# Kernel tuning notes

Hardware: AMD Instinct MI355X
Metric: run time of the kernel (lower is better)

## Reference

```python
import jax, jax.numpy as jnp
import numpy as np

D = 448  # state_dim == input_dim == output_dim

def _param(key, shape):
    # matches torch.rand(shape) * 0.1 + 0.001
    return jax.random.uniform(key, shape, dtype=jnp.float32) * 0.1 + 0.001

def setup_inputs() -> dict:
    key = jax.random.key(0)
    ks = jax.random.split(key, 9)
    x = jax.random.normal(ks[0], (8, 4096, D), dtype=jnp.float32)
    return {
        "x": x,
        "W_q": _param(ks[1], (D, D)),
        "W_k": _param(ks[2], (D, D)),
        "W_v": _param(ks[3], (D, D)),
        "W_o": _param(ks[4], (D, D)),
        "SSM_A": _param(ks[5], (D, D)),
        "SSM_B": _param(ks[6], (D, D)),
        "SSM_C": _param(ks[7], (D, D)),
    }

def reference(x, W_q, W_k, W_v, W_o, SSM_A, SSM_B, SSM_C):
    # seq_len=4096 > threshold=256 -> quadratic SSM path.
    # structured_processing's einsum 'bsd,dd->bsd' multiplies elementwise by
    # the diagonal of the matrix; the block loop is redundant, so we apply the
    # diagonal scale over the whole sequence in one fused op.
    q = jnp.einsum('bsi,id->bsd', x, W_q)
    k = jnp.einsum('bsi,id->bsd', x, W_k)
    v = jnp.einsum('bsi,id->bsd', x, W_v)
    ssm = (q * jnp.diagonal(SSM_A)
           + k * jnp.diagonal(SSM_B)
           + v * jnp.diagonal(SSM_C))
    # dropout is identity in eval mode
    return jnp.einsum('bsd,do->bso', ssm, W_o)
```

## Files before the change

### kernel.cpp

```cpp
#include <hip/hip_runtime.h>
#include <hip/hip_bf16.h>

#define DDIM 448
#define NSTEP 14

typedef __hip_bfloat16 bf16;
typedef __attribute__((ext_vector_type(8))) short short8;
typedef __attribute__((ext_vector_type(4))) float f32x4;

__device__ __forceinline__ short bf_bits(float f) {
    bf16 h = __float2bfloat16(f);
    return *reinterpret_cast<short*>(&h);
}

__device__ __forceinline__ void async16(const bf16* g, bf16* l) {
    __builtin_amdgcn_global_load_lds(
        (const __attribute__((address_space(1))) void*)g,
        (__attribute__((address_space(3))) void*)l, 16, 0, 0);
}

__global__ __launch_bounds__(256) void prep_wc(
    const float* __restrict__ Wq, const float* __restrict__ Wk,
    const float* __restrict__ Wv, const float* __restrict__ Wo,
    const float* __restrict__ Ad, const float* __restrict__ Bd,
    const float* __restrict__ Cd, bf16* __restrict__ Wt)
{
    __shared__ __align__(16) bf16 As[64 * 32];
    __shared__ __align__(16) bf16 Bs[64 * 32];
    __shared__ float da[DDIM], db[DDIM], dc[DDIM];

    const int tid  = threadIdx.x;
    const int i0   = blockIdx.x * 64;
    const int o0   = blockIdx.y * 64;
    const int lane = tid & 63;
    const int wid  = tid >> 6;
    const int wm   = wid >> 1, wn = wid & 1;
    const int m_   = lane & 15, kq = lane >> 4;

    for (int d = tid; d < DDIM; d += 256) {
        da[d] = Ad[d * DDIM + d];
        db[d] = Bd[d * DDIM + d];
        dc[d] = Cd[d * DDIM + d];
    }

    const int dr  = tid >> 3;
    const int oc8 = (tid & 7) * 8;
    const int ir  = tid >> 2;
    const int dc8 = (tid & 3) * 8;

    f32x4 acc[2][2] = {};

    f32x4 w0 = *(const f32x4*)(Wo + dr * DDIM + o0 + oc8);
    f32x4 w1 = *(const f32x4*)(Wo + dr * DDIM + o0 + oc8 + 4);
    f32x4 q0 = *(const f32x4*)(Wq + (i0 + ir) * DDIM + dc8);
    f32x4 q1 = *(const f32x4*)(Wq + (i0 + ir) * DDIM + dc8 + 4);
    f32x4 t0 = *(const f32x4*)(Wk + (i0 + ir) * DDIM + dc8);
    f32x4 t1 = *(const f32x4*)(Wk + (i0 + ir) * DDIM + dc8 + 4);
    f32x4 v0 = *(const f32x4*)(Wv + (i0 + ir) * DDIM + dc8);
    f32x4 v1 = *(const f32x4*)(Wv + (i0 + ir) * DDIM + dc8 + 4);

    for (int k0 = 0; k0 < DDIM; k0 += 32) {
        __syncthreads();
        #pragma unroll
        for (int j = 0; j < 4; ++j) {
            As[(oc8 + j) * 32 + dr]     = __float2bfloat16(w0[j]);
            As[(oc8 + 4 + j) * 32 + dr] = __float2bfloat16(w1[j]);
        }
        short8 e;
        #pragma unroll
        for (int j = 0; j < 4; ++j) {
            e[j]     = bf_bits(q0[j] * da[k0 + dc8 + j]
                             + t0[j] * db[k0 + dc8 + j]
                             + v0[j] * dc[k0 + dc8 + j]);
            e[j + 4] = bf_bits(q1[j] * da[k0 + dc8 + 4 + j]
                             + t1[j] * db[k0 + dc8 + 4 + j]
                             + v1[j] * dc[k0 + dc8 + 4 + j]);
        }
        *(short8*)&Bs[ir * 32 + dc8] = e;
        __syncthreads();

        const int kn = (k0 + 32 < DDIM) ? k0 + 32 : 0;
        w0 = *(const f32x4*)(Wo + (kn + dr) * DDIM + o0 + oc8);
        w1 = *(const f32x4*)(Wo + (kn + dr) * DDIM + o0 + oc8 + 4);
        q0 = *(const f32x4*)(Wq + (i0 + ir) * DDIM + kn + dc8);
        q1 = *(const f32x4*)(Wq + (i0 + ir) * DDIM + kn + dc8 + 4);
        t0 = *(const f32x4*)(Wk + (i0 + ir) * DDIM + kn + dc8);
        t1 = *(const f32x4*)(Wk + (i0 + ir) * DDIM + kn + dc8 + 4);
        v0 = *(const f32x4*)(Wv + (i0 + ir) * DDIM + kn + dc8);
        v1 = *(const f32x4*)(Wv + (i0 + ir) * DDIM + kn + dc8 + 4);

        short8 af[2], bfr[2];
        #pragma unroll
        for (int mi = 0; mi < 2; ++mi)
            af[mi] = *(const short8*)&As[(wm * 32 + mi * 16 + m_) * 32 + kq * 8];
        #pragma unroll
        for (int ni = 0; ni < 2; ++ni)
            bfr[ni] = *(const short8*)&Bs[(wn * 32 + ni * 16 + m_) * 32 + kq * 8];
        #pragma unroll
        for (int mi = 0; mi < 2; ++mi)
            #pragma unroll
            for (int ni = 0; ni < 2; ++ni)
                acc[mi][ni] = __builtin_amdgcn_mfma_f32_16x16x32_bf16(
                    af[mi], bfr[ni], acc[mi][ni], 0, 0, 0);
    }

    #pragma unroll
    for (int mi = 0; mi < 2; ++mi)
        #pragma unroll
        for (int ni = 0; ni < 2; ++ni) {
            const int o = o0 + wm * 32 + mi * 16 + kq * 4;
            const int i = i0 + wn * 32 + ni * 16 + m_;
            bf16* dst = Wt + (i >> 5) * (DDIM * 32) + (i & 31);
            #pragma unroll
            for (int r = 0; r < 4; ++r)
                dst[(o + r) * 32] = __float2bfloat16(acc[mi][ni][r]);
        }
}

__global__ __launch_bounds__(256, 1) void gemm_xwc(
    const float* __restrict__ X, const bf16* __restrict__ Wt,
    float* __restrict__ out)
{
    __shared__ __align__(16) char smem[74240];

    const int tid  = threadIdx.x;
    const int lane = tid & 63;
    const int wid  = tid >> 6;
    const int m_   = lane & 15;
    const int kq   = lane >> 4;
    const int row0 = blockIdx.x * 128;

    const int ar = tid >> 1;
    const int ac = (tid & 1) * 16;
    const float* agp = X + (row0 + ar) * DDIM + ac;

    const bf16* bgp = Wt + wid * 7 * 512 + lane * 8;

    f32x4 acc[8][7] = {};

    {
        bf16* B0 = (bf16*)(smem + 16384);
        #pragma unroll
        for (int j = 0; j < 7; ++j)
            async16(bgp + j * 512, B0 + (wid * 7 + j) * 512);
    }

    f32x4 a0 = *(const f32x4*)(agp);
    f32x4 a1 = *(const f32x4*)(agp + 4);
    f32x4 a2 = *(const f32x4*)(agp + 8);
    f32x4 a3 = *(const f32x4*)(agp + 12);
    {
        bf16* A0 = (bf16*)smem;
        short8 w0, w1;
        #pragma unroll
        for (int j = 0; j < 4; ++j) {
            w0[j] = bf_bits(a0[j]); w0[j + 4] = bf_bits(a1[j]);
            w1[j] = bf_bits(a2[j]); w1[j + 4] = bf_bits(a3[j]);
        }
        *(short8*)&A0[ar * 32 + ac]     = w0;
        *(short8*)&A0[ar * 32 + ac + 8] = w1;
    }
    a0 = *(const f32x4*)(agp + 32);
    a1 = *(const f32x4*)(agp + 36);
    a2 = *(const f32x4*)(agp + 40);
    a3 = *(const f32x4*)(agp + 44);
    __syncthreads();

    for (int s = 0; s < NSTEP; ++s) {
        const int cur = s & 1, nxt = cur ^ 1;
        const bf16* Ac = (const bf16*)(smem + (cur << 13));
        const bf16* Bc = (const bf16*)(smem + 16384 + cur * 28672);

        if (s + 1 < NSTEP) {
            bf16* An = (bf16*)(smem + (nxt << 13));
            bf16* Bn = (bf16*)(smem + 16384 + nxt * 28672);
            short8 w0, w1;
            #pragma unroll
            for (int j = 0; j < 4; ++j) {
                w0[j] = bf_bits(a0[j]); w0[j + 4] = bf_bits(a1[j]);
                w1[j] = bf_bits(a2[j]); w1[j + 4] = bf_bits(a3[j]);
            }
            *(short8*)&An[ar * 32 + ac]     = w0;
            *(short8*)&An[ar * 32 + ac + 8] = w1;
            const bf16* bsrc = bgp + (s + 1) * (DDIM * 32);
            #pragma unroll
            for (int j = 0; j < 7; ++j)
                async16(bsrc + j * 512, Bn + (wid * 7 + j) * 512);
            if (s + 2 < NSTEP) {
                const int k2 = (s + 2) * 32;
                a0 = *(const f32x4*)(agp + k2);
                a1 = *(const f32x4*)(agp + k2 + 4);
                a2 = *(const f32x4*)(agp + k2 + 8);
                a3 = *(const f32x4*)(agp + k2 + 12);
            }
        }

        short8 af[8], bfr[7];
        #pragma unroll
        for (int mi = 0; mi < 8; ++mi)
            af[mi] = *(const short8*)&Ac[(mi * 16 + m_) * 32 + kq * 8];
        #pragma unroll
        for (int ni = 0; ni < 7; ++ni)
            bfr[ni] = *(const short8*)&Bc[(wid * 112 + ni * 16 + m_) * 32 + kq * 8];

        #pragma unroll
        for (int mi = 0; mi < 8; ++mi)
            #pragma unroll
            for (int ni = 0; ni < 7; ++ni)
                acc[mi][ni] = __builtin_amdgcn_mfma_f32_16x16x32_bf16(
                    af[mi], bfr[ni], acc[mi][ni], 0, 0, 0);

        __syncthreads();
    }

    float* Cb = (float*)(smem + 16384);
    #pragma unroll
    for (int t = 0; t < 4; ++t) {
        #pragma unroll
        for (int mi2 = 0; mi2 < 2; ++mi2) {
            const int mi = t * 2 + mi2;
            #pragma unroll
            for (int ni = 0; ni < 7; ++ni) {
                const int col = wid * 112 + ni * 16 + m_;
                #pragma unroll
                for (int r = 0; r < 4; ++r)
                    Cb[(mi2 * 16 + kq * 4 + r) * 452 + col] = acc[mi][ni][r];
            }
        }
        __syncthreads();
        const f32x4* Cb4 = (const f32x4*)Cb;
        f32x4* dst4 = (f32x4*)(out + (row0 + t * 32) * DDIM);
        #pragma unroll
        for (int j = 0; j < 14; ++j) {
            const int v   = j * 256 + tid;
            const int row = v / 112;
            const int cw  = v - row * 112;
            dst4[v] = Cb4[row * 113 + cw];
        }
        __syncthreads();
    }
}

extern "C" void kernel_launch(void* const* d_in, const int* in_sizes, int n_in,
                              void* d_out, int out_size, void* d_ws, size_t ws_size,
                              hipStream_t stream) {
    const float* x  = (const float*)d_in[0];
    const float* Wq = (const float*)d_in[1];
    const float* Wk = (const float*)d_in[2];
    const float* Wv = (const float*)d_in[3];
    const float* Wo = (const float*)d_in[4];
    const float* Ad = (const float*)d_in[5];
    const float* Bd = (const float*)d_in[6];
    const float* Cd = (const float*)d_in[7];

    bf16*  Wt  = (bf16*)d_ws;
    float* out = (float*)d_out;

    const int M = in_sizes[0] / DDIM;

    prep_wc<<<dim3(7, 7), 256, 0, stream>>>(Wq, Wk, Wv, Wo, Ad, Bd, Cd, Wt);
    gemm_xwc<<<M / 128, 256, 0, stream>>>(x, Wt, out);
}
```

Measured before the change: 145.1 us.

## Split GEMM tile across 8 waves with 512-thread blocks

```diff
diff --git a/kernel.cpp b/kernel.cpp
--- a/kernel.cpp
+++ b/kernel.cpp
@@ -117,7 +117,7 @@
         }
 }
 
-__global__ __launch_bounds__(256, 1) void gemm_xwc(
+__global__ __launch_bounds__(512, 2) void gemm_xwc(
     const float* __restrict__ X, const bf16* __restrict__ Wt,
     float* __restrict__ out)
 {
@@ -126,44 +126,42 @@
     const int tid  = threadIdx.x;
     const int lane = tid & 63;
     const int wid  = tid >> 6;
+    const int wr   = wid >> 2;
+    const int wc   = wid & 3;
     const int m_   = lane & 15;
     const int kq   = lane >> 4;
     const int row0 = blockIdx.x * 128;
 
-    const int ar = tid >> 1;
-    const int ac = (tid & 1) * 16;
+    const int ar = tid >> 2;
+    const int ac = (tid & 3) * 8;
     const float* agp = X + (row0 + ar) * DDIM + ac;
 
-    const bf16* bgp = Wt + wid * 7 * 512 + lane * 8;
-
-    f32x4 acc[8][7] = {};
+    const bf16* bgp = Wt + wc * 7 * 512 + lane * 8;
+
+    f32x4 acc[4][7] = {};
 
     {
         bf16* B0 = (bf16*)(smem + 16384);
-        #pragma unroll
-        for (int j = 0; j < 7; ++j)
-            async16(bgp + j * 512, B0 + (wid * 7 + j) * 512);
+        if (wid < 4) {
+            #pragma unroll
+            for (int j = 0; j < 7; ++j)
+                async16(bgp + j * 512, B0 + (wc * 7 + j) * 512);
+        }
     }
 
     f32x4 a0 = *(const f32x4*)(agp);
     f32x4 a1 = *(const f32x4*)(agp + 4);
-    f32x4 a2 = *(const f32x4*)(agp + 8);
-    f32x4 a3 = *(const f32x4*)(agp + 12);
     {
         bf16* A0 = (bf16*)smem;
-        short8 w0, w1;
+        short8 w;
         #pragma unroll
         for (int j = 0; j < 4; ++j) {
-            w0[j] = bf_bits(a0[j]); w0[j + 4] = bf_bits(a1[j]);
-            w1[j] = bf_bits(a2[j]); w1[j + 4] = bf_bits(a3[j]);
-        }
-        *(short8*)&A0[ar * 32 + ac]     = w0;
-        *(short8*)&A0[ar * 32 + ac + 8] = w1;
+            w[j] = bf_bits(a0[j]); w[j + 4] = bf_bits(a1[j]);
+        }
+        *(short8*)&A0[ar * 32 + ac] = w;
     }
     a0 = *(const f32x4*)(agp + 32);
     a1 = *(const f32x4*)(agp + 36);
-    a2 = *(const f32x4*)(agp + 40);
-    a3 = *(const f32x4*)(agp + 44);
     __syncthreads();
 
     for (int s = 0; s < NSTEP; ++s) {
@@ -174,37 +172,35 @@
         if (s + 1 < NSTEP) {
             bf16* An = (bf16*)(smem + (nxt << 13));
             bf16* Bn = (bf16*)(smem + 16384 + nxt * 28672);
-            short8 w0, w1;
+            short8 w;
             #pragma unroll
             for (int j = 0; j < 4; ++j) {
-                w0[j] = bf_bits(a0[j]); w0[j + 4] = bf_bits(a1[j]);
-                w1[j] = bf_bits(a2[j]); w1[j + 4] = bf_bits(a3[j]);
-            }
-            *(short8*)&An[ar * 32 + ac]     = w0;
-            *(short8*)&An[ar * 32 + ac + 8] = w1;
-            const bf16* bsrc = bgp + (s + 1) * (DDIM * 32);
-            #pragma unroll
-            for (int j = 0; j < 7; ++j)
-                async16(bsrc + j * 512, Bn + (wid * 7 + j) * 512);
+                w[j] = bf_bits(a0[j]); w[j + 4] = bf_bits(a1[j]);
+            }
+            *(short8*)&An[ar * 32 + ac] = w;
+            if (wid < 4) {
+                const bf16* bsrc = bgp + (s + 1) * (DDIM * 32);
+                #pragma unroll
+                for (int j = 0; j < 7; ++j)
+                    async16(bsrc + j * 512, Bn + (wc * 7 + j) * 512);
+            }
             if (s + 2 < NSTEP) {
                 const int k2 = (s + 2) * 32;
                 a0 = *(const f32x4*)(agp + k2);
                 a1 = *(const f32x4*)(agp + k2 + 4);
-                a2 = *(const f32x4*)(agp + k2 + 8);
-                a3 = *(const f32x4*)(agp + k2 + 12);
-            }
-        }
-
-        short8 af[8], bfr[7];
-        #pragma unroll
-        for (int mi = 0; mi < 8; ++mi)
-            af[mi] = *(const short8*)&Ac[(mi * 16 + m_) * 32 + kq * 8];
+            }
+        }
+
+        short8 af[4], bfr[7];
+        #pragma unroll
+        for (int mi = 0; mi < 4; ++mi)
+            af[mi] = *(const short8*)&Ac[(wr * 64 + mi * 16 + m_) * 32 + kq * 8];
         #pragma unroll
         for (int ni = 0; ni < 7; ++ni)
-            bfr[ni] = *(const short8*)&Bc[(wid * 112 + ni * 16 + m_) * 32 + kq * 8];
-
-        #pragma unroll
-        for (int mi = 0; mi < 8; ++mi)
+            bfr[ni] = *(const short8*)&Bc[(wc * 112 + ni * 16 + m_) * 32 + kq * 8];
+
+        #pragma unroll
+        for (int mi = 0; mi < 4; ++mi)
             #pragma unroll
             for (int ni = 0; ni < 7; ++ni)
                 acc[mi][ni] = __builtin_amdgcn_mfma_f32_16x16x32_bf16(
@@ -216,23 +212,25 @@
     float* Cb = (float*)(smem + 16384);
     #pragma unroll
     for (int t = 0; t < 4; ++t) {
-        #pragma unroll
-        for (int mi2 = 0; mi2 < 2; ++mi2) {
-            const int mi = t * 2 + mi2;
-            #pragma unroll
-            for (int ni = 0; ni < 7; ++ni) {
-                const int col = wid * 112 + ni * 16 + m_;
+        if (wr == (t >> 1)) {
+            #pragma unroll
+            for (int mi2 = 0; mi2 < 2; ++mi2) {
+                const int mi = (t & 1) * 2 + mi2;
                 #pragma unroll
-                for (int r = 0; r < 4; ++r)
-                    Cb[(mi2 * 16 + kq * 4 + r) * 452 + col] = acc[mi][ni][r];
+                for (int ni = 0; ni < 7; ++ni) {
+                    const int col = wc * 112 + ni * 16 + m_;
+                    #pragma unroll
+                    for (int r = 0; r < 4; ++r)
+                        Cb[(mi2 * 16 + kq * 4 + r) * 452 + col] = acc[mi][ni][r];
+                }
             }
         }
         __syncthreads();
         const f32x4* Cb4 = (const f32x4*)Cb;
         f32x4* dst4 = (f32x4*)(out + (row0 + t * 32) * DDIM);
         #pragma unroll
-        for (int j = 0; j < 14; ++j) {
-            const int v   = j * 256 + tid;
+        for (int j = 0; j < 7; ++j) {
+            const int v   = j * 512 + tid;
             const int row = v / 112;
             const int cw  = v - row * 112;
             dst4[v] = Cb4[row * 113 + cw];
@@ -259,5 +257,5 @@
     const int M = in_sizes[0] / DDIM;
 
     prep_wc<<<dim3(7, 7), 256, 0, stream>>>(Wq, Wk, Wv, Wo, Ad, Bd, Cd, Wt);
-    gemm_xwc<<<M / 128, 256, 0, stream>>>(x, Wt, out);
-}
+    gemm_xwc<<<M / 128, 512, 0, stream>>>(x, Wt, out);
+}
```

Measured after the change: 142.8 us. About the same (-1.6%).
